# Performance work log

Measured on AMD Instinct MI355X. Metric: run time of the kernel, lower is better.

## Reference

```python
import jax, jax.numpy as jnp
import numpy as np

B, IN, HID, OUT, E, K = 16384, 512, 1024, 512, 16, 4


def setup_inputs() -> dict:
    key = jax.random.key(0)
    k0, k1, k2, k3 = jax.random.split(key, 4)
    return {
        "x": jax.random.normal(k0, (B, IN), jnp.float32),
        "w_gate": jax.random.normal(k1, (IN, E), jnp.float32) * 0.02,
        "w1": jax.random.normal(k2, (E, IN, HID), jnp.float32) * (1.0 / np.sqrt(IN)),
        "b1": jnp.zeros((E, HID), jnp.float32),
        "w2": jax.random.normal(k3, (E, HID, OUT), jnp.float32) * (1.0 / np.sqrt(HID)),
        "b2": jnp.zeros((E, OUT), jnp.float32),
    }


def _top_k_gating(x, w_gate):
    # Eval-mode (no noise) noisy_top_k_gating: logits -> top-(k+1) -> softmax over top-k
    logits = x @ w_gate  # [B, E]
    m = min(K + 1, E)
    top_logits, top_idx = jax.lax.top_k(logits, m)  # [B, m]
    tk_logits = top_logits[:, :K]                    # [B, K]
    tk_idx = top_idx[:, :K]                          # [B, K] int32
    tk_gates = jax.nn.softmax(tk_logits, axis=1)     # softmax over the k selected
    rows = jnp.arange(logits.shape[0])[:, None]
    gates = jnp.zeros_like(logits).at[rows, tk_idx].set(tk_gates)  # sparse [B, E]
    return gates


def reference(x, w_gate, w1, b1, w2, b2):
    # Gating
    gates = _top_k_gating(x, w_gate)  # [B, E], zero for non-selected experts
    # Dispatch/combine: output[b] = sum_e gates[b,e] * MLP_e(x[b]).
    # Torch code only evaluates experts on selected rows; since gates are exactly
    # zero elsewhere, the dense weighted sum below computes identical math.
    y = jnp.zeros((x.shape[0], w2.shape[2]), x.dtype)
    for e in range(E):  # fixed small expert count; each iter is one grouped GEMM pair
        h = jax.nn.relu(x @ w1[e] + b1[e])                 # [B, HID]
        o = jax.nn.softmax(h @ w2[e] + b2[e], axis=1)      # expert MLP ends in Softmax(dim=1)
        y = y + gates[:, e:e + 1] * o
    return y
```

## Files before the change

### kernel.cpp

```cpp
#include <hip/hip_runtime.h>
#include <hip/hip_fp16.h>

typedef _Float16 f16;
typedef _Float16 f16x8 __attribute__((ext_vector_type(8)));
typedef float f32x4 __attribute__((ext_vector_type(4)));

#define MFMA(a,b,c) __builtin_amdgcn_mfma_f32_16x16x32_f16((a),(b),(c),0,0,0)

#define BAR() do { \
  asm volatile("s_waitcnt lgkmcnt(0)" ::: "memory"); \
  __builtin_amdgcn_sched_barrier(0); \
  __builtin_amdgcn_s_barrier(); \
  __builtin_amdgcn_sched_barrier(0); \
} while (0)


__global__ void k_cvt_w1(const float* __restrict__ w1, f16* __restrict__ w1fr) {
  int fid = blockIdx.x * 4 + (threadIdx.x >> 6);
  int l = threadIdx.x & 63;
  int e = fid >> 10, n0 = (fid >> 4) & 63, kc = fid & 15;
  int kbase = kc * 32 + (l >> 4) * 8;
  int col = n0 * 16 + (l & 15);
  const float* src = w1 + ((size_t)e * 512 + kbase) * 1024 + col;
  f16x8 o;
  #pragma unroll
  for (int i = 0; i < 8; i++) o[i] = (f16)src[(size_t)i * 1024];
  *(f16x8*)(w1fr + (size_t)fid * 512 + l * 8) = o;
}

__global__ void k_cvt_w2(const float* __restrict__ w2, f16* __restrict__ w2fr) {
  int fid = blockIdx.x * 4 + (threadIdx.x >> 6);
  int l = threadIdx.x & 63;
  int e = fid >> 10, n0 = (fid >> 5) & 31, kc = fid & 31;
  int kbase = kc * 32 + (l >> 4) * 8;
  int col = n0 * 16 + (l & 15);
  const float* src = w2 + ((size_t)e * 1024 + kbase) * 512 + col;
  f16x8 o;
  #pragma unroll
  for (int i = 0; i < 8; i++) o[i] = (f16)src[(size_t)i * 512];
  *(f16x8*)(w2fr + (size_t)fid * 512 + l * 8) = o;
}

__global__ void k_gate(const float* __restrict__ x, const float* __restrict__ wg,
                       int* __restrict__ tk_idx, float* __restrict__ tk_gate) {
  int w = threadIdx.x >> 6, l = threadIdx.x & 63;
  int r = blockIdx.x * 4 + w;
  float p[16];
  #pragma unroll
  for (int e = 0; e < 16; e++) p[e] = 0.f;
  const float* xr = x + (size_t)r * 512;
  #pragma unroll
  for (int t = 0; t < 8; t++) {
    float xv = xr[t * 64 + l];
    const float* wrow = wg + (t * 64 + l) * 16;
    #pragma unroll
    for (int e = 0; e < 16; e++) p[e] += xv * wrow[e];
  }
  #pragma unroll
  for (int e = 0; e < 16; e++) {
    float v = p[e];
    #pragma unroll
    for (int m = 32; m >= 1; m >>= 1) v += __shfl_xor(v, m);
    p[e] = v;
  }
  unsigned chosen = 0;
  float bv[4]; int bi[4];
  #pragma unroll
  for (int j = 0; j < 4; j++) {
    float best = -3.4e38f; int be = 0;
    #pragma unroll
    for (int e = 0; e < 16; e++) {
      bool ok = !((chosen >> e) & 1u) && (p[e] > best);
      if (ok) { best = p[e]; be = e; }
    }
    chosen |= 1u << be; bv[j] = best; bi[j] = be;
  }
  float m0 = bv[0];
  float e0 = __expf(bv[0] - m0), e1 = __expf(bv[1] - m0),
        e2 = __expf(bv[2] - m0), e3 = __expf(bv[3] - m0);
  float s = e0 + e1 + e2 + e3;
  if (l == 0) {
    *(int4*)(tk_idx + (size_t)r * 4) = make_int4(bi[0], bi[1], bi[2], bi[3]);
    *(float4*)(tk_gate + (size_t)r * 4) = make_float4(e0 / s, e1 / s, e2 / s, e3 / s);
  }
}

__global__ void k_route_count(const int* __restrict__ tk_idx, int* __restrict__ partial) {
  int e = blockIdx.x >> 6, chunk = blockIdx.x & 63;
  int t = threadIdx.x;
  int row = chunk * 256 + t;
  int4 tk = ((const int4*)tk_idx)[row];
  bool match = (tk.x == e) || (tk.y == e) || (tk.z == e) || (tk.w == e);
  unsigned long long m = __ballot(match);
  __shared__ int wc[4];
  if ((t & 63) == 0) wc[t >> 6] = (int)__popcll(m);
  __syncthreads();
  if (t == 0) partial[e * 64 + chunk] = wc[0] + wc[1] + wc[2] + wc[3];
}

__global__ void k_route_scan(const int* __restrict__ partial, int* __restrict__ chunk_base,
                             int* __restrict__ count) {
  int l = threadIdx.x;
  for (int e = 0; e < 16; e++) {
    int v = partial[e * 64 + l];
    int orig = v;
    #pragma unroll
    for (int off = 1; off < 64; off <<= 1) {
      int u = __shfl_up(v, off);
      if (l >= off) v += u;
    }
    chunk_base[e * 64 + l] = v - orig;
    if (l == 63) count[e] = v;
  }
}

__global__ void k_route_scatter(const int* __restrict__ tk_idx, const float* __restrict__ tk_gate,
                                const int* __restrict__ chunk_base, int* __restrict__ rows_pk,
                                float* __restrict__ gates_l) {
  int e = blockIdx.x >> 6, chunk = blockIdx.x & 63;
  int t = threadIdx.x, w = t >> 6, l = t & 63;
  int row = chunk * 256 + t;
  int4 tk = ((const int4*)tk_idx)[row];
  int j = (tk.x == e) ? 0 : (tk.y == e) ? 1 : (tk.z == e) ? 2 : (tk.w == e) ? 3 : -1;
  bool match = (j >= 0);
  unsigned long long m = __ballot(match);
  __shared__ int wc[4];
  if (l == 0) wc[w] = (int)__popcll(m);
  __syncthreads();
  int wbase = 0;
  #pragma unroll
  for (int i = 0; i < 4; i++) if (i < w) wbase += wc[i];
  if (match) {
    int pos = (int)__popcll(m & ((1ULL << l) - 1ULL));
    int idx = e * 16384 + chunk_base[e * 64 + chunk] + wbase + pos;
    rows_pk[idx] = row | (j << 16);
    gates_l[idx] = tk_gate[(size_t)row * 4 + j];
  }
}

__global__ void k_zero(float4* __restrict__ y4) {
  y4[blockIdx.x * 256 + threadIdx.x] = make_float4(0.f, 0.f, 0.f, 0.f);
}

__global__ __launch_bounds__(1024, 4) void k_expert(
    const float* __restrict__ x, const f16* __restrict__ w1fr, const f16* __restrict__ w2fr,
    const float* __restrict__ b1, const float* __restrict__ b2,
    const int* __restrict__ count, const int* __restrict__ rows_pk,
    const float* __restrict__ gates_l, float* __restrict__ y)
{
  int p = blockIdx.x;
  int xcd = p & 7, s = p >> 3;
  int e = (xcd << 1) | (s >> 8);
  int rb = s & 255;
  int cnt = count[e];
  int mstart = rb * 64;
  if (mstart >= cnt) return;
  int nvalid = cnt - mstart; if (nvalid > 64) nvalid = 64;

  __shared__ f16 x_lds[64 * 512];
  __shared__ f16 h_lds[64 * 256];
  __shared__ int rowarr[64];
  __shared__ float gatearr[64];
  __shared__ float red[2][16][64];

  int t = threadIdx.x, w = t >> 6, l = t & 63;
  int lq = l >> 4, lr = l & 15;

  if (t < 64) {
    int idx = (t < nvalid) ? t : (nvalid - 1);
    int src = e * 16384 + mstart + idx;
    rowarr[t] = rows_pk[src];
    gatearr[t] = gates_l[src];
  }
  BAR();

  {
    int rX = t >> 4, s0 = t & 15;
    const float* sp = x + (size_t)(rowarr[rX] & 0xFFFF) * 512;
    char* xb = (char*)x_lds;
    #pragma unroll
    for (int j = 0; j < 4; j++) {
      int seg = s0 + j * 16;
      const float* qp = sp + seg * 8;
      float4 u0 = ((const float4*)qp)[0], u1 = ((const float4*)qp)[1];
      f16x8 v;
      v[0]=(f16)u0.x; v[1]=(f16)u0.y; v[2]=(f16)u0.z; v[3]=(f16)u0.w;
      v[4]=(f16)u1.x; v[5]=(f16)u1.y; v[6]=(f16)u1.z; v[7]=(f16)u1.w;
      int byte = rX * 1024 + ((seg ^ rX) & 63) * 16;
      *(f16x8*)(xb + byte) = v;
    }
  }
  BAR();

  const f16x8* w1f8 = (const f16x8*)w1fr;
  const f16x8* w2f8 = (const f16x8*)w2fr;
  char* xb = (char*)x_lds;
  char* hb = (char*)h_lds;

  f32x4 acc2[4][2];
  #pragma unroll
  for (int a = 0; a < 4; a++)
    #pragma unroll
    for (int b = 0; b < 2; b++)
      #pragma unroll
      for (int q = 0; q < 4; q++) acc2[a][b][q] = 0.f;

  #pragma unroll 1
  for (int hc = 0; hc < 4; hc++) {
    f32x4 acc1[4];
    #pragma unroll
    for (int a = 0; a < 4; a++)
      #pragma unroll
      for (int q = 0; q < 4; q++) acc1[a][q] = 0.f;

    const f16x8* bp1 = w1f8 + ((size_t)((e * 64 + hc * 16 + w) * 16)) * 64 + l;
    #pragma unroll 4
    for (int kcg = 0; kcg < 16; kcg++) {
      f16x8 bf = bp1[kcg * 64];
      int seg = kcg * 4 + lq;
      #pragma unroll
      for (int mf = 0; mf < 4; mf++) {
        int row = mf * 16 + lr;
        f16x8 av = *(const f16x8*)(xb + row * 1024 + ((seg ^ row) & 63) * 16);
        acc1[mf] = MFMA(av, bf, acc1[mf]);
      }
    }

    BAR();
    {
      int cc = w * 16 + lr;
      float bv = b1[e * 1024 + hc * 256 + cc];
      int seg = w * 2 + (lr >> 3);
      #pragma unroll
      for (int mf = 0; mf < 4; mf++)
        #pragma unroll
        for (int q = 0; q < 4; q++) {
          int row = mf * 16 + lq * 4 + q;
          float hv = fmaxf(acc1[mf][q] + bv, 0.f);
          int byte = row * 512 + ((seg ^ row) & 31) * 16 + (lr & 7) * 2;
          *(f16*)(hb + byte) = (f16)hv;
        }
    }
    BAR();

    const f16x8* bp2a = w2f8 + ((size_t)((e * 32 + w * 2) * 32 + hc * 8)) * 64 + l;
    const f16x8* bp2b = bp2a + (size_t)32 * 64;
    #pragma unroll 2
    for (int kc2 = 0; kc2 < 8; kc2++) {
      f16x8 wf0 = bp2a[kc2 * 64];
      f16x8 wf1 = bp2b[kc2 * 64];
      int seg = kc2 * 4 + lq;
      #pragma unroll
      for (int mf = 0; mf < 4; mf++) {
        int row = mf * 16 + lr;
        f16x8 av = *(const f16x8*)(hb + row * 512 + ((seg ^ row) & 31) * 16);
        acc2[mf][0] = MFMA(av, wf0, acc2[mf][0]);
        acc2[mf][1] = MFMA(av, wf1, acc2[mf][1]);
      }
    }
  }

  #pragma unroll
  for (int nf = 0; nf < 2; nf++) {
    float bv = b2[e * 512 + w * 32 + nf * 16 + lr];
    #pragma unroll
    for (int mf = 0; mf < 4; mf++)
      #pragma unroll
      for (int q = 0; q < 4; q++) acc2[mf][nf][q] += bv;
  }

  float rmax[4][4];
  #pragma unroll
  for (int mf = 0; mf < 4; mf++)
    #pragma unroll
    for (int q = 0; q < 4; q++) {
      float v = fmaxf(acc2[mf][0][q], acc2[mf][1][q]);
      #pragma unroll
      for (int m = 1; m < 16; m <<= 1) v = fmaxf(v, __shfl_xor(v, m));
      rmax[mf][q] = v;
    }
  if (lr == 0) {
    #pragma unroll
    for (int mf = 0; mf < 4; mf++)
      #pragma unroll
      for (int q = 0; q < 4; q++) red[0][w][mf * 16 + lq * 4 + q] = rmax[mf][q];
  }
  BAR();
  float gmax[4][4];
  #pragma unroll
  for (int mf = 0; mf < 4; mf++)
    #pragma unroll
    for (int q = 0; q < 4; q++) {
      int row = mf * 16 + lq * 4 + q;
      float v = red[0][0][row];
      #pragma unroll
      for (int ww = 1; ww < 16; ww++) v = fmaxf(v, red[0][ww][row]);
      gmax[mf][q] = v;
    }
  float psum[4][4];
  #pragma unroll
  for (int mf = 0; mf < 4; mf++)
    #pragma unroll
    for (int q = 0; q < 4; q++) psum[mf][q] = 0.f;
  #pragma unroll
  for (int mf = 0; mf < 4; mf++)
    #pragma unroll
    for (int nf = 0; nf < 2; nf++)
      #pragma unroll
      for (int q = 0; q < 4; q++) {
        float pp = __expf(acc2[mf][nf][q] - gmax[mf][q]);
        acc2[mf][nf][q] = pp;
        psum[mf][q] += pp;
      }
  #pragma unroll
  for (int mf = 0; mf < 4; mf++)
    #pragma unroll
    for (int q = 0; q < 4; q++) {
      float v = psum[mf][q];
      #pragma unroll
      for (int m = 1; m < 16; m <<= 1) v += __shfl_xor(v, m);
      psum[mf][q] = v;
    }
  if (lr == 0) {
    #pragma unroll
    for (int mf = 0; mf < 4; mf++)
      #pragma unroll
      for (int q = 0; q < 4; q++) red[1][w][mf * 16 + lq * 4 + q] = psum[mf][q];
  }
  BAR();

  #pragma unroll
  for (int mf = 0; mf < 4; mf++) {
    #pragma unroll
    for (int q = 0; q < 4; q++) {
      int row = mf * 16 + lq * 4 + q;
      if (row < nvalid) {
        float ssum = 0.f;
        #pragma unroll
        for (int ww = 0; ww < 16; ww++) ssum += red[1][ww][row];
        float sc = gatearr[row] / ssum;
        int orow = rowarr[row] & 0xFFFF;
        float* yr = y + (size_t)orow * 512 + w * 32 + lr;
        atomicAdd(yr, acc2[mf][0][q] * sc);
        atomicAdd(yr + 16, acc2[mf][1][q] * sc);
      }
    }
  }
}

extern "C" void kernel_launch(void* const* d_in, const int* in_sizes, int n_in,
                              void* d_out, int out_size, void* d_ws, size_t ws_size,
                              hipStream_t stream) {
  (void)in_sizes; (void)n_in; (void)out_size; (void)ws_size;
  const float* x  = (const float*)d_in[0];
  const float* wg = (const float*)d_in[1];
  const float* w1 = (const float*)d_in[2];
  const float* b1 = (const float*)d_in[3];
  const float* w2 = (const float*)d_in[4];
  const float* b2 = (const float*)d_in[5];
  float* y = (float*)d_out;

  char* ws = (char*)d_ws;
  size_t off = 0;
  auto alloc = [&](size_t bytes) -> char* {
    char* p = ws + off;
    off += (bytes + 255) & ~(size_t)255;
    return p;
  };
  f16*   w1fr       = (f16*)  alloc((size_t)16 * 512 * 1024 * 2);
  f16*   w2fr       = (f16*)  alloc((size_t)16 * 1024 * 512 * 2);
  int*   tk_idx     = (int*)  alloc((size_t)16384 * 4 * 4);
  float* tk_gate    = (float*)alloc((size_t)16384 * 4 * 4);
  int*   rows_pk    = (int*)  alloc((size_t)16 * 16384 * 4);
  float* gates_l    = (float*)alloc((size_t)16 * 16384 * 4);
  int*   partial    = (int*)  alloc(16 * 64 * 4);
  int*   chunk_base = (int*)  alloc(16 * 64 * 4);
  int*   count      = (int*)  alloc(256);

  k_cvt_w1<<<dim3(4096), dim3(256), 0, stream>>>(w1, w1fr);
  k_cvt_w2<<<dim3(4096), dim3(256), 0, stream>>>(w2, w2fr);
  k_gate<<<dim3(4096), dim3(256), 0, stream>>>(x, wg, tk_idx, tk_gate);
  k_route_count<<<dim3(1024), dim3(256), 0, stream>>>(tk_idx, partial);
  k_route_scan<<<dim3(1), dim3(64), 0, stream>>>(partial, chunk_base, count);
  k_route_scatter<<<dim3(1024), dim3(256), 0, stream>>>(tk_idx, tk_gate, chunk_base,
                                                        rows_pk, gates_l);
  k_zero<<<dim3(8192), dim3(256), 0, stream>>>((float4*)y);
  k_expert<<<dim3(4096), dim3(1024), 0, stream>>>(x, w1fr, w2fr, b1, b2,
                                                  count, rows_pk, gates_l, y);
}
```

Measured before the change: 410.0 us.

## Double expert row tile to 128 and reload x per hidden chunk into shared buffer

```diff
diff --git a/kernel.cpp b/kernel.cpp
--- a/kernel.cpp
+++ b/kernel.cpp
@@ -142,7 +142,7 @@
   y4[blockIdx.x * 256 + threadIdx.x] = make_float4(0.f, 0.f, 0.f, 0.f);
 }
 
-__global__ __launch_bounds__(1024, 4) void k_expert(
+__global__ __launch_bounds__(1024, 1) void k_expert(
     const float* __restrict__ x, const f16* __restrict__ w1fr, const f16* __restrict__ w2fr,
     const float* __restrict__ b1, const float* __restrict__ b2,
     const int* __restrict__ count, const int* __restrict__ rows_pk,
@@ -150,56 +150,29 @@
 {
   int p = blockIdx.x;
   int xcd = p & 7, s = p >> 3;
-  int e = (xcd << 1) | (s >> 8);
-  int rb = s & 255;
+  int e = (xcd << 1) | (s >> 7);
+  int rb = s & 127;
   int cnt = count[e];
-  int mstart = rb * 64;
+  int mstart = rb * 128;
   if (mstart >= cnt) return;
-  int nvalid = cnt - mstart; if (nvalid > 64) nvalid = 64;
-
-  __shared__ f16 x_lds[64 * 512];
-  __shared__ f16 h_lds[64 * 256];
-  __shared__ int rowarr[64];
-  __shared__ float gatearr[64];
-  __shared__ float red[2][16][64];
+  int nvalid = cnt - mstart; if (nvalid > 128) nvalid = 128;
+
+  __shared__ char buf[131072];
+  __shared__ float red[2][16][128];
 
   int t = threadIdx.x, w = t >> 6, l = t & 63;
   int lq = l >> 4, lr = l & 15;
 
-  if (t < 64) {
-    int idx = (t < nvalid) ? t : (nvalid - 1);
-    int src = e * 16384 + mstart + idx;
-    rowarr[t] = rows_pk[src];
-    gatearr[t] = gates_l[src];
-  }
-  BAR();
-
-  {
-    int rX = t >> 4, s0 = t & 15;
-    const float* sp = x + (size_t)(rowarr[rX] & 0xFFFF) * 512;
-    char* xb = (char*)x_lds;
-    #pragma unroll
-    for (int j = 0; j < 4; j++) {
-      int seg = s0 + j * 16;
-      const float* qp = sp + seg * 8;
-      float4 u0 = ((const float4*)qp)[0], u1 = ((const float4*)qp)[1];
-      f16x8 v;
-      v[0]=(f16)u0.x; v[1]=(f16)u0.y; v[2]=(f16)u0.z; v[3]=(f16)u0.w;
-      v[4]=(f16)u1.x; v[5]=(f16)u1.y; v[6]=(f16)u1.z; v[7]=(f16)u1.w;
-      int byte = rX * 1024 + ((seg ^ rX) & 63) * 16;
-      *(f16x8*)(xb + byte) = v;
-    }
-  }
-  BAR();
+  int srow = t >> 3, s0 = t & 7;
+  int sidx = e * 16384 + mstart + ((srow < nvalid) ? srow : (nvalid - 1));
+  const float* sp = x + (size_t)(rows_pk[sidx] & 0xFFFF) * 512;
 
   const f16x8* w1f8 = (const f16x8*)w1fr;
   const f16x8* w2f8 = (const f16x8*)w2fr;
-  char* xb = (char*)x_lds;
-  char* hb = (char*)h_lds;
-
-  f32x4 acc2[4][2];
-  #pragma unroll
-  for (int a = 0; a < 4; a++)
+
+  f32x4 acc2[8][2];
+  #pragma unroll
+  for (int a = 0; a < 8; a++)
     #pragma unroll
     for (int b = 0; b < 2; b++)
       #pragma unroll
@@ -207,21 +180,38 @@
 
   #pragma unroll 1
   for (int hc = 0; hc < 4; hc++) {
-    f32x4 acc1[4];
-    #pragma unroll
-    for (int a = 0; a < 4; a++)
+    BAR();
+    {
+      #pragma unroll
+      for (int j = 0; j < 8; j++) {
+        int seg = s0 + j * 8;
+        const f32x4* qp = (const f32x4*)(sp + seg * 8);
+        f32x4 u0 = __builtin_nontemporal_load(qp);
+        f32x4 u1 = __builtin_nontemporal_load(qp + 1);
+        f16x8 v;
+        v[0]=(f16)u0[0]; v[1]=(f16)u0[1]; v[2]=(f16)u0[2]; v[3]=(f16)u0[3];
+        v[4]=(f16)u1[0]; v[5]=(f16)u1[1]; v[6]=(f16)u1[2]; v[7]=(f16)u1[3];
+        int byte = srow * 1024 + ((seg ^ srow) & 63) * 16;
+        *(f16x8*)(buf + byte) = v;
+      }
+    }
+    BAR();
+
+    f32x4 acc1[8];
+    #pragma unroll
+    for (int a = 0; a < 8; a++)
       #pragma unroll
       for (int q = 0; q < 4; q++) acc1[a][q] = 0.f;
 
     const f16x8* bp1 = w1f8 + ((size_t)((e * 64 + hc * 16 + w) * 16)) * 64 + l;
-    #pragma unroll 4
+    #pragma unroll 2
     for (int kcg = 0; kcg < 16; kcg++) {
       f16x8 bf = bp1[kcg * 64];
       int seg = kcg * 4 + lq;
       #pragma unroll
-      for (int mf = 0; mf < 4; mf++) {
+      for (int mf = 0; mf < 8; mf++) {
         int row = mf * 16 + lr;
-        f16x8 av = *(const f16x8*)(xb + row * 1024 + ((seg ^ row) & 63) * 16);
+        f16x8 av = *(const f16x8*)(buf + row * 1024 + ((seg ^ row) & 63) * 16);
         acc1[mf] = MFMA(av, bf, acc1[mf]);
       }
     }
@@ -232,13 +222,13 @@
       float bv = b1[e * 1024 + hc * 256 + cc];
       int seg = w * 2 + (lr >> 3);
       #pragma unroll
-      for (int mf = 0; mf < 4; mf++)
+      for (int mf = 0; mf < 8; mf++)
         #pragma unroll
         for (int q = 0; q < 4; q++) {
           int row = mf * 16 + lq * 4 + q;
           float hv = fmaxf(acc1[mf][q] + bv, 0.f);
           int byte = row * 512 + ((seg ^ row) & 31) * 16 + (lr & 7) * 2;
-          *(f16*)(hb + byte) = (f16)hv;
+          *(f16*)(buf + byte) = (f16)hv;
         }
     }
     BAR();
@@ -251,9 +241,9 @@
       f16x8 wf1 = bp2b[kc2 * 64];
       int seg = kc2 * 4 + lq;
       #pragma unroll
-      for (int mf = 0; mf < 4; mf++) {
+      for (int mf = 0; mf < 8; mf++) {
         int row = mf * 16 + lr;
-        f16x8 av = *(const f16x8*)(hb + row * 512 + ((seg ^ row) & 31) * 16);
+        f16x8 av = *(const f16x8*)(buf + row * 512 + ((seg ^ row) & 31) * 16);
         acc2[mf][0] = MFMA(av, wf0, acc2[mf][0]);
         acc2[mf][1] = MFMA(av, wf1, acc2[mf][1]);
       }
@@ -264,73 +254,44 @@
   for (int nf = 0; nf < 2; nf++) {
     float bv = b2[e * 512 + w * 32 + nf * 16 + lr];
     #pragma unroll
-    for (int mf = 0; mf < 4; mf++)
+    for (int mf = 0; mf < 8; mf++)
       #pragma unroll
       for (int q = 0; q < 4; q++) acc2[mf][nf][q] += bv;
   }
 
-  float rmax[4][4];
-  #pragma unroll
-  for (int mf = 0; mf < 4; mf++)
+  #pragma unroll
+  for (int mf = 0; mf < 8; mf++) {
     #pragma unroll
     for (int q = 0; q < 4; q++) {
       float v = fmaxf(acc2[mf][0][q], acc2[mf][1][q]);
       #pragma unroll
       for (int m = 1; m < 16; m <<= 1) v = fmaxf(v, __shfl_xor(v, m));
-      rmax[mf][q] = v;
-    }
-  if (lr == 0) {
-    #pragma unroll
-    for (int mf = 0; mf < 4; mf++)
-      #pragma unroll
-      for (int q = 0; q < 4; q++) red[0][w][mf * 16 + lq * 4 + q] = rmax[mf][q];
+      if (lr == 0) red[0][w][mf * 16 + lq * 4 + q] = v;
+    }
   }
   BAR();
-  float gmax[4][4];
-  #pragma unroll
-  for (int mf = 0; mf < 4; mf++)
+  #pragma unroll 2
+  for (int mf = 0; mf < 8; mf++) {
     #pragma unroll
     for (int q = 0; q < 4; q++) {
       int row = mf * 16 + lq * 4 + q;
-      float v = red[0][0][row];
-      #pragma unroll
-      for (int ww = 1; ww < 16; ww++) v = fmaxf(v, red[0][ww][row]);
-      gmax[mf][q] = v;
-    }
-  float psum[4][4];
-  #pragma unroll
-  for (int mf = 0; mf < 4; mf++)
-    #pragma unroll
-    for (int q = 0; q < 4; q++) psum[mf][q] = 0.f;
-  #pragma unroll
-  for (int mf = 0; mf < 4; mf++)
-    #pragma unroll
-    for (int nf = 0; nf < 2; nf++)
-      #pragma unroll
-      for (int q = 0; q < 4; q++) {
-        float pp = __expf(acc2[mf][nf][q] - gmax[mf][q]);
-        acc2[mf][nf][q] = pp;
-        psum[mf][q] += pp;
-      }
-  #pragma unroll
-  for (int mf = 0; mf < 4; mf++)
-    #pragma unroll
-    for (int q = 0; q < 4; q++) {
-      float v = psum[mf][q];
+      float g = red[0][0][row];
+      #pragma unroll
+      for (int ww = 1; ww < 16; ww++) g = fmaxf(g, red[0][ww][row]);
+      float p0 = __expf(acc2[mf][0][q] - g);
+      float p1 = __expf(acc2[mf][1][q] - g);
+      acc2[mf][0][q] = p0;
+      acc2[mf][1][q] = p1;
+      float v = p0 + p1;
       #pragma unroll
       for (int m = 1; m < 16; m <<= 1) v += __shfl_xor(v, m);
-      psum[mf][q] = v;
-    }
-  if (lr == 0) {
-    #pragma unroll
-    for (int mf = 0; mf < 4; mf++)
-      #pragma unroll
-      for (int q = 0; q < 4; q++) red[1][w][mf * 16 + lq * 4 + q] = psum[mf][q];
+      if (lr == 0) red[1][w][row] = v;
+    }
   }
   BAR();
 
-  #pragma unroll
-  for (int mf = 0; mf < 4; mf++) {
+  #pragma unroll 2
+  for (int mf = 0; mf < 8; mf++) {
     #pragma unroll
     for (int q = 0; q < 4; q++) {
       int row = mf * 16 + lq * 4 + q;
@@ -338,8 +299,10 @@
         float ssum = 0.f;
         #pragma unroll
         for (int ww = 0; ww < 16; ww++) ssum += red[1][ww][row];
-        float sc = gatearr[row] / ssum;
-        int orow = rowarr[row] & 0xFFFF;
+        int gidx = e * 16384 + mstart + row;
+        int code = rows_pk[gidx];
+        float sc = gates_l[gidx] / ssum;
+        int orow = code & 0xFFFF;
         float* yr = y + (size_t)orow * 512 + w * 32 + lr;
         atomicAdd(yr, acc2[mf][0][q] * sc);
         atomicAdd(yr + 16, acc2[mf][1][q] * sc);
@@ -385,6 +348,6 @@
   k_route_scatter<<<dim3(1024), dim3(256), 0, stream>>>(tk_idx, tk_gate, chunk_base,
                                                         rows_pk, gates_l);
   k_zero<<<dim3(8192), dim3(256), 0, stream>>>((float4*)y);
-  k_expert<<<dim3(4096), dim3(1024), 0, stream>>>(x, w1fr, w2fr, b1, b2,
+  k_expert<<<dim3(2048), dim3(1024), 0, stream>>>(x, w1fr, w2fr, b1, b2,
                                                   count, rows_pk, gates_l, y);
 }
```

After: 750.9 us. 1.83x slower.

## Halve expert-kernel waves, widen per-wave N tile to 64 columns

Applied to the files above, without the earlier changes.

```diff
diff --git a/kernel.cpp b/kernel.cpp
--- a/kernel.cpp
+++ b/kernel.cpp
@@ -142,7 +142,7 @@
   y4[blockIdx.x * 256 + threadIdx.x] = make_float4(0.f, 0.f, 0.f, 0.f);
 }
 
-__global__ __launch_bounds__(1024, 4) void k_expert(
+__global__ __launch_bounds__(512, 2) void k_expert(
     const float* __restrict__ x, const f16* __restrict__ w1fr, const f16* __restrict__ w2fr,
     const float* __restrict__ b1, const float* __restrict__ b2,
     const int* __restrict__ count, const int* __restrict__ rows_pk,
@@ -158,10 +158,10 @@
   int nvalid = cnt - mstart; if (nvalid > 64) nvalid = 64;
 
   __shared__ f16 x_lds[64 * 512];
-  __shared__ f16 h_lds[64 * 256];
+  __shared__ f16 h_lds[64 * 512];
   __shared__ int rowarr[64];
   __shared__ float gatearr[64];
-  __shared__ float red[2][16][64];
+  __shared__ float red[2][8][64];
 
   int t = threadIdx.x, w = t >> 6, l = t & 63;
   int lq = l >> 4, lr = l & 15;
@@ -174,19 +174,21 @@
   }
   BAR();
 
+  char* xb = (char*)x_lds;
+  char* hb = (char*)h_lds;
+
   {
-    int rX = t >> 4, s0 = t & 15;
-    const float* sp = x + (size_t)(rowarr[rX] & 0xFFFF) * 512;
-    char* xb = (char*)x_lds;
-    #pragma unroll
-    for (int j = 0; j < 4; j++) {
-      int seg = s0 + j * 16;
+    int srow = t >> 3, sj = t & 7;
+    const float* sp = x + (size_t)(rowarr[srow] & 0xFFFF) * 512;
+    #pragma unroll
+    for (int j = 0; j < 8; j++) {
+      int seg = sj + j * 8;
       const float* qp = sp + seg * 8;
       float4 u0 = ((const float4*)qp)[0], u1 = ((const float4*)qp)[1];
       f16x8 v;
       v[0]=(f16)u0.x; v[1]=(f16)u0.y; v[2]=(f16)u0.z; v[3]=(f16)u0.w;
       v[4]=(f16)u1.x; v[5]=(f16)u1.y; v[6]=(f16)u1.z; v[7]=(f16)u1.w;
-      int byte = rX * 1024 + ((seg ^ rX) & 63) * 16;
+      int byte = srow * 1024 + ((seg ^ srow) & 63) * 16;
       *(f16x8*)(xb + byte) = v;
     }
   }
@@ -194,75 +196,94 @@
 
   const f16x8* w1f8 = (const f16x8*)w1fr;
   const f16x8* w2f8 = (const f16x8*)w2fr;
-  char* xb = (char*)x_lds;
-  char* hb = (char*)h_lds;
-
-  f32x4 acc2[4][2];
+
+  f32x4 acc2[4][4];
   #pragma unroll
   for (int a = 0; a < 4; a++)
     #pragma unroll
-    for (int b = 0; b < 2; b++)
+    for (int b = 0; b < 4; b++)
       #pragma unroll
       for (int q = 0; q < 4; q++) acc2[a][b][q] = 0.f;
 
   #pragma unroll 1
-  for (int hc = 0; hc < 4; hc++) {
-    f32x4 acc1[4];
+  for (int hc = 0; hc < 2; hc++) {
+    f32x4 acc1[4][4];
     #pragma unroll
     for (int a = 0; a < 4; a++)
       #pragma unroll
-      for (int q = 0; q < 4; q++) acc1[a][q] = 0.f;
-
-    const f16x8* bp1 = w1f8 + ((size_t)((e * 64 + hc * 16 + w) * 16)) * 64 + l;
+      for (int b = 0; b < 4; b++)
+        #pragma unroll
+        for (int q = 0; q < 4; q++) acc1[a][b][q] = 0.f;
+
+    const f16x8* bp1 = w1f8 + ((size_t)((e * 64 + hc * 32 + w * 4) * 16)) * 64 + l;
     #pragma unroll 4
     for (int kcg = 0; kcg < 16; kcg++) {
-      f16x8 bf = bp1[kcg * 64];
+      f16x8 bf0 = bp1[kcg * 64];
+      f16x8 bf1 = bp1[16 * 64 + kcg * 64];
+      f16x8 bf2 = bp1[32 * 64 + kcg * 64];
+      f16x8 bf3 = bp1[48 * 64 + kcg * 64];
       int seg = kcg * 4 + lq;
+      f16x8 av[4];
       #pragma unroll
       for (int mf = 0; mf < 4; mf++) {
         int row = mf * 16 + lr;
-        f16x8 av = *(const f16x8*)(xb + row * 1024 + ((seg ^ row) & 63) * 16);
-        acc1[mf] = MFMA(av, bf, acc1[mf]);
+        av[mf] = *(const f16x8*)(xb + row * 1024 + ((seg ^ row) & 63) * 16);
+      }
+      #pragma unroll
+      for (int mf = 0; mf < 4; mf++) {
+        acc1[mf][0] = MFMA(av[mf], bf0, acc1[mf][0]);
+        acc1[mf][1] = MFMA(av[mf], bf1, acc1[mf][1]);
+        acc1[mf][2] = MFMA(av[mf], bf2, acc1[mf][2]);
+        acc1[mf][3] = MFMA(av[mf], bf3, acc1[mf][3]);
       }
     }
 
     BAR();
-    {
-      int cc = w * 16 + lr;
-      float bv = b1[e * 1024 + hc * 256 + cc];
-      int seg = w * 2 + (lr >> 3);
+    #pragma unroll
+    for (int nf = 0; nf < 4; nf++) {
+      int cc = w * 64 + nf * 16 + lr;
+      float bv = b1[e * 1024 + hc * 512 + cc];
+      int segw = cc >> 3;
+      int inb = (cc & 7) * 2;
       #pragma unroll
       for (int mf = 0; mf < 4; mf++)
         #pragma unroll
         for (int q = 0; q < 4; q++) {
           int row = mf * 16 + lq * 4 + q;
-          float hv = fmaxf(acc1[mf][q] + bv, 0.f);
-          int byte = row * 512 + ((seg ^ row) & 31) * 16 + (lr & 7) * 2;
+          float hv = fmaxf(acc1[mf][nf][q] + bv, 0.f);
+          int byte = row * 1024 + ((segw ^ row) & 63) * 16 + inb;
           *(f16*)(hb + byte) = (f16)hv;
         }
     }
     BAR();
 
-    const f16x8* bp2a = w2f8 + ((size_t)((e * 32 + w * 2) * 32 + hc * 8)) * 64 + l;
-    const f16x8* bp2b = bp2a + (size_t)32 * 64;
-    #pragma unroll 2
-    for (int kc2 = 0; kc2 < 8; kc2++) {
-      f16x8 wf0 = bp2a[kc2 * 64];
-      f16x8 wf1 = bp2b[kc2 * 64];
+    const f16x8* bp2 = w2f8 + ((size_t)((e * 32 + w * 4) * 32 + hc * 16)) * 64 + l;
+    #pragma unroll 4
+    for (int kc2 = 0; kc2 < 16; kc2++) {
+      f16x8 wf0 = bp2[kc2 * 64];
+      f16x8 wf1 = bp2[32 * 64 + kc2 * 64];
+      f16x8 wf2 = bp2[64 * 64 + kc2 * 64];
+      f16x8 wf3 = bp2[96 * 64 + kc2 * 64];
       int seg = kc2 * 4 + lq;
+      f16x8 av[4];
       #pragma unroll
       for (int mf = 0; mf < 4; mf++) {
         int row = mf * 16 + lr;
-        f16x8 av = *(const f16x8*)(hb + row * 512 + ((seg ^ row) & 31) * 16);
-        acc2[mf][0] = MFMA(av, wf0, acc2[mf][0]);
-        acc2[mf][1] = MFMA(av, wf1, acc2[mf][1]);
-      }
-    }
-  }
-
-  #pragma unroll
-  for (int nf = 0; nf < 2; nf++) {
-    float bv = b2[e * 512 + w * 32 + nf * 16 + lr];
+        av[mf] = *(const f16x8*)(hb + row * 1024 + ((seg ^ row) & 63) * 16);
+      }
+      #pragma unroll
+      for (int mf = 0; mf < 4; mf++) {
+        acc2[mf][0] = MFMA(av[mf], wf0, acc2[mf][0]);
+        acc2[mf][1] = MFMA(av[mf], wf1, acc2[mf][1]);
+        acc2[mf][2] = MFMA(av[mf], wf2, acc2[mf][2]);
+        acc2[mf][3] = MFMA(av[mf], wf3, acc2[mf][3]);
+      }
+    }
+  }
+
+  #pragma unroll
+  for (int nf = 0; nf < 4; nf++) {
+    float bv = b2[e * 512 + w * 64 + nf * 16 + lr];
     #pragma unroll
     for (int mf = 0; mf < 4; mf++)
       #pragma unroll
@@ -274,7 +295,9 @@
   for (int mf = 0; mf < 4; mf++)
     #pragma unroll
     for (int q = 0; q < 4; q++) {
-      float v = fmaxf(acc2[mf][0][q], acc2[mf][1][q]);
+      float v = acc2[mf][0][q];
+      #pragma unroll
+      for (int nf = 1; nf < 4; nf++) v = fmaxf(v, acc2[mf][nf][q]);
       #pragma unroll
       for (int m = 1; m < 16; m <<= 1) v = fmaxf(v, __shfl_xor(v, m));
       rmax[mf][q] = v;
@@ -294,7 +317,7 @@
       int row = mf * 16 + lq * 4 + q;
       float v = red[0][0][row];
       #pragma unroll
-      for (int ww = 1; ww < 16; ww++) v = fmaxf(v, red[0][ww][row]);
+      for (int ww = 1; ww < 8; ww++) v = fmaxf(v, red[0][ww][row]);
       gmax[mf][q] = v;
     }
   float psum[4][4];
@@ -305,7 +328,7 @@
   #pragma unroll
   for (int mf = 0; mf < 4; mf++)
     #pragma unroll
-    for (int nf = 0; nf < 2; nf++)
+    for (int nf = 0; nf < 4; nf++)
       #pragma unroll
       for (int q = 0; q < 4; q++) {
         float pp = __expf(acc2[mf][nf][q] - gmax[mf][q]);
@@ -337,12 +360,14 @@
       if (row < nvalid) {
         float ssum = 0.f;
         #pragma unroll
-        for (int ww = 0; ww < 16; ww++) ssum += red[1][ww][row];
+        for (int ww = 0; ww < 8; ww++) ssum += red[1][ww][row];
         float sc = gatearr[row] / ssum;
         int orow = rowarr[row] & 0xFFFF;
-        float* yr = y + (size_t)orow * 512 + w * 32 + lr;
-        atomicAdd(yr, acc2[mf][0][q] * sc);
-        atomicAdd(yr + 16, acc2[mf][1][q] * sc);
+        float* yr = y + (size_t)orow * 512 + w * 64 + lr;
+        #pragma unroll
+        for (int nf = 0; nf < 4; nf++) {
+          atomicAdd(yr + nf * 16, acc2[mf][nf][q] * sc);
+        }
       }
     }
   }
@@ -385,6 +410,6 @@
   k_route_scatter<<<dim3(1024), dim3(256), 0, stream>>>(tk_idx, tk_gate, chunk_base,
                                                         rows_pk, gates_l);
   k_zero<<<dim3(8192), dim3(256), 0, stream>>>((float4*)y);
-  k_expert<<<dim3(4096), dim3(1024), 0, stream>>>(x, w1fr, w2fr, b1, b2,
-                                                  count, rows_pk, gates_l, y);
-}
+  k_expert<<<dim3(4096), dim3(512), 0, stream>>>(x, w1fr, w2fr, b1, b2,
+                                                 count, rows_pk, gates_l, y);
+}
```

Measured after the change: 387.0 us. 5.6% less time.
